# Kernel optimization log

Measured on AMD Instinct MI355X. Metric: run time of the kernel, lower is better.

Reference implementation:

```python
import jax, jax.numpy as jnp
import numpy as np

ALPHA = 0.2  # leaky relu slope


def setup_inputs() -> dict:
    key = jax.random.key(0)
    k_h, k_adj, k_w, k_a = jax.random.split(key, 4)
    B, N, F_in, F_out, H = 4, 2048, 128, 64, 4
    h = jax.random.normal(k_h, (B, N, F_in), dtype=jnp.float32)
    adj = jax.random.randint(k_adj, (N, N), 0, 2).astype(jnp.float32)
    # xavier_uniform with gain=1.414 (as in reset_parameters)
    gain = 1.414
    lim_w = gain * np.sqrt(6.0 / (F_in + F_out))
    W = jax.random.uniform(k_w, (H, F_in, F_out), minval=-lim_w, maxval=lim_w, dtype=jnp.float32)
    lim_a = gain * np.sqrt(6.0 / (2 * F_out + 1))
    a = jax.random.uniform(k_a, (H, 2 * F_out, 1), minval=-lim_a, maxval=lim_a, dtype=jnp.float32)
    return {"h": h, "adj": adj, "W": W, "a": a}


def reference(h, adj, W, a):
    B, N, _ = h.shape
    F_out = W.shape[2]
    # per-head linear transform: [B, N, H, F_out]
    ht = jnp.einsum('hio,bni->bnho', W, h)
    # split attention vector into src/dst halves; a^T [h_i; h_j] = a_src.h_i + a_dst.h_j
    a_src = a[:, :F_out, 0]   # [H, F_out]
    a_dst = a[:, F_out:, 0]   # [H, F_out]
    e_src = jnp.einsum('bnho,ho->bnh', ht, a_src)  # score contribution of node i (rows)
    e_dst = jnp.einsum('bnho,ho->bnh', ht, a_dst)  # score contribution of node j (cols)
    e = e_src[:, :, None, :] + e_dst[:, None, :, :]           # [B, N, N, H]
    e = jnp.where(e >= 0, e, ALPHA * e)                        # leaky relu
    e = e + (-1e20 * (1.0 - adj))[None, :, :, None]            # adjacency mask (shared over batch/heads)
    att = jax.nn.softmax(e, axis=2)                            # softmax over neighbors j
    # dropout p=0.0 (eval-mode reference): identity
    h_prime = jnp.einsum('bmnh,bnho->bmho', att, ht)           # [B, N, H, F_out]
    return h_prime.reshape(B, N, -1)                           # concat heads -> [B, N, H*F_out]
```

## Files before the change

kernel.cpp:

```cpp
#include <hip/hip_runtime.h>

#define ALPHA 0.2f
#define LOG2E 1.44269504088896340736f

constexpr int BB  = 4;
constexpr int NN  = 2048;
constexpr int FIN = 128;
constexpr int FO  = 64;
constexpr int HH  = 4;
constexpr int CC  = BB * HH;

using half8   = __attribute__((ext_vector_type(8))) _Float16;
using floatx4 = __attribute__((ext_vector_type(4))) float;

__device__ __forceinline__ float fast_exp2(float x) {
#if __has_builtin(__builtin_amdgcn_exp2f)
  return __builtin_amdgcn_exp2f(x);
#else
  return exp2f(x);
#endif
}

union PK4 { _Float16 f[4]; uint2 u; };

__global__ __launch_bounds__(256) void gat_k12(
    const float* __restrict__ h, const float* __restrict__ W,
    const float* __restrict__ a, const float* __restrict__ adj,
    _Float16* __restrict__ htT, float* __restrict__ esrcT,
    float* __restrict__ edst, float* __restrict__ gpart,
    unsigned* __restrict__ adjbits) {
  const int blk = blockIdx.x;
  const int t = threadIdx.x;
  const int w = t >> 6, lane = t & 63;

  if (blk < 512) {
    const int m = blk * 4 + w;
    float areg[32];
    const float* arow = adj + (size_t)m * NN;
#pragma unroll
    for (int j = 0; j < 32; ++j) areg[j] = arow[j * 64 + lane];
#pragma unroll
    for (int j = 0; j < 32; ++j) {
      const unsigned long long mask = __ballot(areg[j] != 0.f);
      if (lane == 0) {
        adjbits[m * 64 + j * 2 + 0] = (unsigned)mask;
        adjbits[m * 64 + j * 2 + 1] = (unsigned)(mask >> 32);
      }
    }
    return;
  }

  const int pb = blk - 512;
  const int c  = (pb & 7) | (((pb >> 3) & 1) << 3);
  const int nt = pb >> 4;
  const int n0 = nt * 64;
  const int b = c >> 2, hh = c & 3;
  const int q = lane >> 4, r16 = lane & 15;

  __shared__ __align__(16) _Float16 Xs[64 * 128];
  __shared__ __align__(16) _Float16 WT[64 * 128];
  __shared__ float wasb[128];
  __shared__ float wadb[128];
  __shared__ float edsh[64];

  {
    const int k = t & 127;
    const float* wrow = W + ((size_t)hh * 128 + k) * 64;
    const float* av = a + hh * 128 + ((t >> 7) << 6);
    float s = 0.f;
#pragma unroll
    for (int o = 0; o < 16; ++o) {
      const float4 wv = *(const float4*)(wrow + o * 4);
      const float4 av4 = *(const float4*)(av + o * 4);
      s += wv.x * av4.x + wv.y * av4.y + wv.z * av4.z + wv.w * av4.w;
    }
    if (t < 128) wasb[k] = s; else wadb[k] = s;
  }

  {
    const int k = t >> 1, fh = (t & 1) * 32;
    const float* wsrc = W + ((size_t)hh * 128 + k) * 64 + fh;
    const int chunk = k >> 3, within = k & 7;
#pragma unroll
    for (int i = 0; i < 8; ++i) {
      const float4 v = *(const float4*)(wsrc + i * 4);
      const _Float16 f4[4] = {(_Float16)v.x, (_Float16)v.y,
                              (_Float16)v.z, (_Float16)v.w};
#pragma unroll
      for (int u = 0; u < 4; ++u) {
        const int f = fh + i * 4 + u;
        WT[f * 128 + ((chunk ^ (f & 15)) << 3) + within] = f4[u];
      }
    }
  }

  __syncthreads();

  {
    const int r = t >> 2, cq = t & 3;
    const float* hsrc = h + ((size_t)(b * NN + n0 + r)) * FIN + cq * 32;
    float es = 0.f, ed = 0.f;
#pragma unroll
    for (int i = 0; i < 8; ++i) {
      const float4 v = *(const float4*)(hsrc + i * 4);
      const float4 ws = *(const float4*)&wasb[cq * 32 + i * 4];
      const float4 wd = *(const float4*)&wadb[cq * 32 + i * 4];
      es += v.x * ws.x + v.y * ws.y + v.z * ws.z + v.w * ws.w;
      ed += v.x * wd.x + v.y * wd.y + v.z * wd.z + v.w * wd.w;
      PK4 pk;
      pk.f[0] = (_Float16)v.x; pk.f[1] = (_Float16)v.y;
      pk.f[2] = (_Float16)v.z; pk.f[3] = (_Float16)v.w;
      const int chunk = cq * 4 + (i >> 1);
      *(uint2*)&Xs[r * 128 + ((chunk ^ (r & 15)) << 3) + (i & 1) * 4] = pk.u;
    }
    es += __shfl_xor(es, 1, 64); es += __shfl_xor(es, 2, 64);
    ed += __shfl_xor(ed, 1, 64); ed += __shfl_xor(ed, 2, 64);
    if (cq == 0) {
      const float edl = ed * LOG2E;
      esrcT[(size_t)(n0 + r) * CC + c] = es * LOG2E;
      edst[(size_t)c * NN + n0 + r]    = edl;
      edsh[r] = edl;
    }
  }

  __syncthreads();

  if (t < 64) {
    float v = edsh[t];
#pragma unroll
    for (int off = 1; off < 64; off <<= 1) v = fmaxf(v, __shfl_xor(v, off, 64));
    if (t == 0) gpart[c * 32 + nt] = v;
  }

  floatx4 acc[4];
#pragma unroll
  for (int ft = 0; ft < 4; ++ft) acc[ft] = floatx4{0.f, 0.f, 0.f, 0.f};

  half8 afrag[4];
#pragma unroll
  for (int ks = 0; ks < 4; ++ks) {
    const int slot = (ks * 4 + q) ^ r16;
    afrag[ks] = *(const half8*)&Xs[(w * 16 + r16) * 128 + (slot << 3)];
  }
#pragma unroll
  for (int ks = 0; ks < 4; ++ks) {
#pragma unroll
    for (int ft = 0; ft < 4; ++ft) {
      const int fr = ft * 16 + r16;
      const int slot = (ks * 4 + q) ^ (fr & 15);
      const half8 bfrag = *(const half8*)&WT[fr * 128 + (slot << 3)];
      acc[ft] = __builtin_amdgcn_mfma_f32_16x16x32_f16(afrag[ks], bfrag,
                                                       acc[ft], 0, 0, 0);
    }
  }

#pragma unroll
  for (int ft = 0; ft < 4; ++ft) {
    PK4 pk;
#pragma unroll
    for (int x = 0; x < 4; ++x) pk.f[x] = (_Float16)acc[ft][x];
    const int fcol = ft * 16 + r16;
    const int n = n0 + w * 16 + q * 4;
    *(uint2*)(htT + ((size_t)c * FO + fcol) * NN + n) = pk.u;
  }
}

__global__ __launch_bounds__(1024, 8) void gat_k3_pv(
    const _Float16* __restrict__ htT, const float* __restrict__ esrcT,
    const float* __restrict__ edst, const unsigned* __restrict__ adjbits,
    const float* __restrict__ gpart, float* __restrict__ out) {
  const int blk0 = blockIdx.x;
  const int c  = (blk0 & 7) | (((blk0 >> 3) & 1) << 3);
  const int m0 = (blk0 >> 4) * 64;
  const int b = c >> 2, hh = c & 3;
  const int t = threadIdx.x;
  const int w = t >> 6;
  const int kg = w >> 2;
  const int wl = w & 3;
  const int lane = t & 63;
  const int q = lane >> 4, r16 = lane & 15;
  const int row = m0 + wl * 16 + r16;
  const int rl  = wl * 16 + r16;

  __shared__ __align__(16) char smem[81920];
  _Float16* Vt  = (_Float16*)smem;
  float* zzF    = (float*)(smem + 49152);
  unsigned* abL = (unsigned*)(smem + 65536);
  float* abuf   = (float*)smem;

  const _Float16* vsrc = htT + (size_t)c * FO * NN;

  const int f0 = t >> 4, sg0 = t & 15;
  const size_t goff0 = (size_t)f0 * NN + (size_t)((sg0 ^ (f0 & 15)) * 8);

#define STAGE(BUF, NBASE)                                                      \
  __builtin_amdgcn_global_load_lds(                                            \
      (const __attribute__((address_space(1))) void*)(vsrc + goff0 + (NBASE)), \
      (__attribute__((address_space(3))) void*)(smem + (BUF)*16384 + t*16),    \
      16, 0, 0)

  const float em = esrcT[(size_t)row * CC + c];
  const float2 edv = *(const float2*)(edst + (size_t)c * NN + t * 2);
  const uint4 abv = *(const uint4*)&adjbits[(size_t)(m0 + (t >> 4)) * 64 +
                                            (t & 15) * 4];
  float gv = gpart[c * 32 + (lane & 31)];

  {
    float4 zzv;
    zzv.x = fast_exp2(edv.x);
    zzv.y = fast_exp2(ALPHA * edv.x);
    zzv.z = fast_exp2(edv.y);
    zzv.w = fast_exp2(ALPHA * edv.y);
    *(float4*)&zzF[t * 4] = zzv;
  }
  *(uint4*)&abL[(t >> 4) * 64 + (((t & 15) ^ ((t >> 4) & 15)) << 2)] = abv;

#pragma unroll
  for (int off = 1; off < 32; off <<= 1)
    gv = fmaxf(gv, __shfl_xor(gv, off, 64));
  const float gm = gv;

  __syncthreads();

  const float s0r = em + gm;
  const float rm = (s0r >= 0.f) ? s0r : ALPHA * s0r;
  const float Am   = fast_exp2(em - rm);
  const float Bm   = fast_exp2(fmaf(ALPHA, em, -rm));
  const float Zthr = fast_exp2(-em);

  floatx4 acc[4];
#pragma unroll
  for (int ft = 0; ft < 4; ++ft) acc[ft] = floatx4{0.f, 0.f, 0.f, 0.f};
  floatx4 accs = floatx4{0.f, 0.f, 0.f, 0.f};

  half8 ones;
#pragma unroll
  for (int k = 0; k < 8; ++k) ones[k] = (_Float16)1.0f;

  STAGE(0, 0);
  STAGE(1, 128);

#pragma unroll
  for (int step = 0; step < 16; ++step) {
    const int bufs = step % 3;
    const unsigned bits =
        abL[rl * 64 + ((step ^ (rl & 15)) << 2) + kg] >> (q * 8);
    const int nb = step * 128 + kg * 32 + q * 8;
    float4 vz[4];
#pragma unroll
    for (int i = 0; i < 4; ++i) vz[i] = *(const float4*)&zzF[nb * 2 + i * 4];
    const float* zp = (const float*)vz;
    half8 afrag;
#pragma unroll
    for (int k = 0; k < 8; ++k) {
      const float z1 = zp[2 * k], z2 = zp[2 * k + 1];
      const bool sel = (z1 >= Zthr);
      const float zc = sel ? z1 : z2;
      const float cf = sel ? Am : Bm;
      float p = cf * zc;
      p = ((bits >> k) & 1u) ? p : 0.f;
      afrag[k] = (_Float16)p;
    }

    if (step < 15) {
      asm volatile("s_waitcnt vmcnt(1) lgkmcnt(0)" ::: "memory");
    } else {
      asm volatile("s_waitcnt vmcnt(0) lgkmcnt(0)" ::: "memory");
    }
    __builtin_amdgcn_s_barrier();
    asm volatile("" ::: "memory");

    if (step <= 13) STAGE((step + 2) % 3, (step + 2) * 128);

    const int bufo = bufs * 8192;
    __builtin_amdgcn_s_setprio(1);
    accs = __builtin_amdgcn_mfma_f32_16x16x32_f16(afrag, ones, accs, 0, 0, 0);
#pragma unroll
    for (int ft = 0; ft < 4; ++ft) {
      const int fr = ft * 16 + r16;
      const int oct = kg * 4 + q;
      const half8 bfrag =
          *(const half8*)&Vt[bufo + fr * 128 + ((oct ^ (fr & 15)) << 3)];
      acc[ft] = __builtin_amdgcn_mfma_f32_16x16x32_f16(afrag, bfrag,
                                                       acc[ft], 0, 0, 0);
    }
    __builtin_amdgcn_s_setprio(0);
  }

  __syncthreads();
  if (kg >= 1) {
    const int base = ((kg - 1) * 256 + (t & 255)) * 21;
#pragma unroll
    for (int ft = 0; ft < 4; ++ft)
#pragma unroll
      for (int x = 0; x < 4; ++x) abuf[base + ft * 4 + x] = acc[ft][x];
#pragma unroll
    for (int x = 0; x < 4; ++x) abuf[base + 16 + x] = accs[x];
  }
  __syncthreads();
  if (kg == 0) {
#pragma unroll
    for (int g = 0; g < 3; ++g) {
      const int base = (g * 256 + t) * 21;
#pragma unroll
      for (int ft = 0; ft < 4; ++ft)
#pragma unroll
        for (int x = 0; x < 4; ++x) acc[ft][x] += abuf[base + ft * 4 + x];
#pragma unroll
      for (int x = 0; x < 4; ++x) accs[x] += abuf[base + 16 + x];
    }
#pragma unroll
    for (int x = 0; x < 4; ++x) {
      const float rinv = 1.0f / accs[x];
      const int mrow = m0 + wl * 16 + q * 4 + x;
      float* op = out + ((size_t)b * NN + mrow) * 256 + hh * 64;
#pragma unroll
      for (int ft = 0; ft < 4; ++ft) op[ft * 16 + r16] = acc[ft][x] * rinv;
    }
  }
#undef STAGE
}

extern "C" void kernel_launch(void* const* d_in, const int* in_sizes, int n_in,
                              void* d_out, int out_size, void* d_ws, size_t ws_size,
                              hipStream_t stream) {
  const float* h   = (const float*)d_in[0];
  const float* adj = (const float*)d_in[1];
  const float* W   = (const float*)d_in[2];
  const float* a   = (const float*)d_in[3];
  float* out = (float*)d_out;

  char* ws = (char*)d_ws;
  _Float16* htT   = (_Float16*)(ws);
  float* esrcT    = (float*)(ws + 4 * 1024 * 1024);
  float* edst     = (float*)(ws + 4 * 1024 * 1024 + 131072);
  unsigned* abits = (unsigned*)(ws + 4 * 1024 * 1024 + 2 * 131072);
  float* gpart    = (float*)(ws + 4 * 1024 * 1024 + 2 * 131072 + 524288);

  gat_k12<<<dim3(1024), dim3(256), 0, stream>>>(h, W, a, adj, htT, esrcT,
                                                edst, gpart, abits);
  gat_k3_pv<<<dim3(CC * (NN / 64)), dim3(1024), 0, stream>>>(htT, esrcT, edst,
                                                             abits, gpart, out);
}
```

Before: 108.3 us.

## Fuse projection and attention kernels with a grid-wide atomic barrier

Merges the projection/adjacency-bitmask kernel and the attention PV kernel into one persistent launch of 512 blocks of 1024 threads. Warps 0-3 do the per-tile projection and warps 4-11 pack adjacency bits. A software grid barrier (atomic counter plus spin with sleep) then separates the phases before the attention work. This removes one kernel launch and its tail gap, but adds a memset, relies on all 512 blocks being co-resident, and leaves many threads idle during the first phase.

```diff
diff --git a/kernel.cpp b/kernel.cpp
--- a/kernel.cpp
+++ b/kernel.cpp
@@ -9,6 +9,7 @@
 constexpr int FO  = 64;
 constexpr int HH  = 4;
 constexpr int CC  = BB * HH;
+constexpr unsigned NBLK = 512;
 
 using half8   = __attribute__((ext_vector_type(8))) _Float16;
 using floatx4 = __attribute__((ext_vector_type(4))) float;
@@ -23,80 +24,83 @@
 
 union PK4 { _Float16 f[4]; uint2 u; };
 
-__global__ __launch_bounds__(256) void gat_k12(
+__global__ __launch_bounds__(1024, 8) void gat_fused(
     const float* __restrict__ h, const float* __restrict__ W,
     const float* __restrict__ a, const float* __restrict__ adj,
     _Float16* __restrict__ htT, float* __restrict__ esrcT,
     float* __restrict__ edst, float* __restrict__ gpart,
-    unsigned* __restrict__ adjbits) {
-  const int blk = blockIdx.x;
+    unsigned* __restrict__ adjbits, unsigned* __restrict__ bar,
+    float* __restrict__ out) {
+  const int blk0 = blockIdx.x;
+  const int c    = (blk0 & 7) | (((blk0 >> 3) & 1) << 3);
+  const int tile = blk0 >> 4;
+  const int b = c >> 2, hh = c & 3;
   const int t = threadIdx.x;
-  const int w = t >> 6, lane = t & 63;
-
-  if (blk < 512) {
-    const int m = blk * 4 + w;
-    float areg[32];
+  const int lane = t & 63;
+  const int q = lane >> 4, r16 = lane & 15;
+  const int n0 = tile * 64;
+
+  __shared__ __align__(16) char smem[81920];
+  _Float16* Xs  = (_Float16*)smem;
+  _Float16* WT  = (_Float16*)(smem + 16384);
+  float* wasb   = (float*)(smem + 32768);
+  float* wadb   = (float*)(smem + 33280);
+  float* edsh   = (float*)(smem + 33792);
+
+  if (t < 256) {
+    {
+      const int k = t & 127;
+      const float* wrow = W + ((size_t)hh * 128 + k) * 64;
+      const float* av = a + hh * 128 + ((t >> 7) << 6);
+      float s = 0.f;
+#pragma unroll
+      for (int o = 0; o < 16; ++o) {
+        const float4 wv = *(const float4*)(wrow + o * 4);
+        const float4 av4 = *(const float4*)(av + o * 4);
+        s += wv.x * av4.x + wv.y * av4.y + wv.z * av4.z + wv.w * av4.w;
+      }
+      if (t < 128) wasb[k] = s; else wadb[k] = s;
+    }
+    {
+      const int k = t >> 1, fh = (t & 1) * 32;
+      const float* wsrc = W + ((size_t)hh * 128 + k) * 64 + fh;
+      const int chunk = k >> 3, within = k & 7;
+#pragma unroll
+      for (int i = 0; i < 8; ++i) {
+        const float4 v = *(const float4*)(wsrc + i * 4);
+        const _Float16 f4[4] = {(_Float16)v.x, (_Float16)v.y,
+                                (_Float16)v.z, (_Float16)v.w};
+#pragma unroll
+        for (int u = 0; u < 4; ++u) {
+          const int f = fh + i * 4 + u;
+          WT[f * 128 + ((chunk ^ (f & 15)) << 3) + within] = f4[u];
+        }
+      }
+    }
+  } else if (t < 768) {
+    const int tb = t - 256;
+    const int wv = tb >> 6;
+    const int rowi = wv >> 1;
+    const int jb = (wv & 1) * 16;
+    const int l = tb & 63;
+    const int m = blk0 * 4 + rowi;
     const float* arow = adj + (size_t)m * NN;
-#pragma unroll
-    for (int j = 0; j < 32; ++j) areg[j] = arow[j * 64 + lane];
-#pragma unroll
-    for (int j = 0; j < 32; ++j) {
+    float areg[16];
+#pragma unroll
+    for (int j = 0; j < 16; ++j) areg[j] = arow[(jb + j) * 64 + l];
+#pragma unroll
+    for (int j = 0; j < 16; ++j) {
       const unsigned long long mask = __ballot(areg[j] != 0.f);
-      if (lane == 0) {
-        adjbits[m * 64 + j * 2 + 0] = (unsigned)mask;
-        adjbits[m * 64 + j * 2 + 1] = (unsigned)(mask >> 32);
+      if (l == 0) {
+        adjbits[m * 64 + (jb + j) * 2 + 0] = (unsigned)mask;
+        adjbits[m * 64 + (jb + j) * 2 + 1] = (unsigned)(mask >> 32);
       }
     }
-    return;
-  }
-
-  const int pb = blk - 512;
-  const int c  = (pb & 7) | (((pb >> 3) & 1) << 3);
-  const int nt = pb >> 4;
-  const int n0 = nt * 64;
-  const int b = c >> 2, hh = c & 3;
-  const int q = lane >> 4, r16 = lane & 15;
-
-  __shared__ __align__(16) _Float16 Xs[64 * 128];
-  __shared__ __align__(16) _Float16 WT[64 * 128];
-  __shared__ float wasb[128];
-  __shared__ float wadb[128];
-  __shared__ float edsh[64];
-
-  {
-    const int k = t & 127;
-    const float* wrow = W + ((size_t)hh * 128 + k) * 64;
-    const float* av = a + hh * 128 + ((t >> 7) << 6);
-    float s = 0.f;
-#pragma unroll
-    for (int o = 0; o < 16; ++o) {
-      const float4 wv = *(const float4*)(wrow + o * 4);
-      const float4 av4 = *(const float4*)(av + o * 4);
-      s += wv.x * av4.x + wv.y * av4.y + wv.z * av4.z + wv.w * av4.w;
-    }
-    if (t < 128) wasb[k] = s; else wadb[k] = s;
-  }
-
-  {
-    const int k = t >> 1, fh = (t & 1) * 32;
-    const float* wsrc = W + ((size_t)hh * 128 + k) * 64 + fh;
-    const int chunk = k >> 3, within = k & 7;
-#pragma unroll
-    for (int i = 0; i < 8; ++i) {
-      const float4 v = *(const float4*)(wsrc + i * 4);
-      const _Float16 f4[4] = {(_Float16)v.x, (_Float16)v.y,
-                              (_Float16)v.z, (_Float16)v.w};
-#pragma unroll
-      for (int u = 0; u < 4; ++u) {
-        const int f = fh + i * 4 + u;
-        WT[f * 128 + ((chunk ^ (f & 15)) << 3) + within] = f4[u];
-      }
-    }
-  }
-
-  __syncthreads();
-
-  {
+  }
+
+  __syncthreads();
+
+  if (t < 256) {
     const int r = t >> 2, cq = t & 3;
     const float* hsrc = h + ((size_t)(b * NN + n0 + r)) * FIN + cq * 32;
     float es = 0.f, ed = 0.f;
@@ -129,60 +133,61 @@
     float v = edsh[t];
 #pragma unroll
     for (int off = 1; off < 64; off <<= 1) v = fmaxf(v, __shfl_xor(v, off, 64));
-    if (t == 0) gpart[c * 32 + nt] = v;
-  }
-
-  floatx4 acc[4];
-#pragma unroll
-  for (int ft = 0; ft < 4; ++ft) acc[ft] = floatx4{0.f, 0.f, 0.f, 0.f};
-
-  half8 afrag[4];
-#pragma unroll
-  for (int ks = 0; ks < 4; ++ks) {
-    const int slot = (ks * 4 + q) ^ r16;
-    afrag[ks] = *(const half8*)&Xs[(w * 16 + r16) * 128 + (slot << 3)];
-  }
-#pragma unroll
-  for (int ks = 0; ks < 4; ++ks) {
+    if (t == 0) gpart[c * 32 + tile] = v;
+  }
+  if (t < 256) {
+    const int w1 = t >> 6;
+    floatx4 pacc[4];
+#pragma unroll
+    for (int ft = 0; ft < 4; ++ft) pacc[ft] = floatx4{0.f, 0.f, 0.f, 0.f};
+    half8 pafrag[4];
+#pragma unroll
+    for (int ks = 0; ks < 4; ++ks) {
+      const int slot = (ks * 4 + q) ^ r16;
+      pafrag[ks] = *(const half8*)&Xs[(w1 * 16 + r16) * 128 + (slot << 3)];
+    }
+#pragma unroll
+    for (int ks = 0; ks < 4; ++ks) {
+#pragma unroll
+      for (int ft = 0; ft < 4; ++ft) {
+        const int fr = ft * 16 + r16;
+        const int slot = (ks * 4 + q) ^ (fr & 15);
+        const half8 bfrag = *(const half8*)&WT[fr * 128 + (slot << 3)];
+        pacc[ft] = __builtin_amdgcn_mfma_f32_16x16x32_f16(pafrag[ks], bfrag,
+                                                          pacc[ft], 0, 0, 0);
+      }
+    }
 #pragma unroll
     for (int ft = 0; ft < 4; ++ft) {
-      const int fr = ft * 16 + r16;
-      const int slot = (ks * 4 + q) ^ (fr & 15);
-      const half8 bfrag = *(const half8*)&WT[fr * 128 + (slot << 3)];
-      acc[ft] = __builtin_amdgcn_mfma_f32_16x16x32_f16(afrag[ks], bfrag,
-                                                       acc[ft], 0, 0, 0);
-    }
-  }
-
-#pragma unroll
-  for (int ft = 0; ft < 4; ++ft) {
-    PK4 pk;
-#pragma unroll
-    for (int x = 0; x < 4; ++x) pk.f[x] = (_Float16)acc[ft][x];
-    const int fcol = ft * 16 + r16;
-    const int n = n0 + w * 16 + q * 4;
-    *(uint2*)(htT + ((size_t)c * FO + fcol) * NN + n) = pk.u;
-  }
-}
-
-__global__ __launch_bounds__(1024, 8) void gat_k3_pv(
-    const _Float16* __restrict__ htT, const float* __restrict__ esrcT,
-    const float* __restrict__ edst, const unsigned* __restrict__ adjbits,
-    const float* __restrict__ gpart, float* __restrict__ out) {
-  const int blk0 = blockIdx.x;
-  const int c  = (blk0 & 7) | (((blk0 >> 3) & 1) << 3);
-  const int m0 = (blk0 >> 4) * 64;
-  const int b = c >> 2, hh = c & 3;
-  const int t = threadIdx.x;
+      PK4 pk;
+#pragma unroll
+      for (int x = 0; x < 4; ++x) pk.f[x] = (_Float16)pacc[ft][x];
+      const int fcol = ft * 16 + r16;
+      const int n = n0 + w1 * 16 + q * 4;
+      *(uint2*)(htT + ((size_t)c * FO + fcol) * NN + n) = pk.u;
+    }
+  }
+
+  __syncthreads();
+  if (t == 0) {
+    __hip_atomic_fetch_add(bar, 1u, __ATOMIC_RELEASE,
+                           __HIP_MEMORY_SCOPE_AGENT);
+    unsigned v;
+    do {
+      __builtin_amdgcn_s_sleep(8);
+      v = __hip_atomic_load(bar, __ATOMIC_RELAXED, __HIP_MEMORY_SCOPE_AGENT);
+    } while (v < NBLK);
+  }
+  __syncthreads();
+  __builtin_amdgcn_fence(__ATOMIC_ACQUIRE, "agent");
+
+  const int m0 = tile * 64;
   const int w = t >> 6;
   const int kg = w >> 2;
   const int wl = w & 3;
-  const int lane = t & 63;
-  const int q = lane >> 4, r16 = lane & 15;
   const int row = m0 + wl * 16 + r16;
   const int rl  = wl * 16 + r16;
 
-  __shared__ __align__(16) char smem[81920];
   _Float16* Vt  = (_Float16*)smem;
   float* zzF    = (float*)(smem + 49152);
   unsigned* abL = (unsigned*)(smem + 65536);
@@ -336,9 +341,9 @@
   float* edst     = (float*)(ws + 4 * 1024 * 1024 + 131072);
   unsigned* abits = (unsigned*)(ws + 4 * 1024 * 1024 + 2 * 131072);
   float* gpart    = (float*)(ws + 4 * 1024 * 1024 + 2 * 131072 + 524288);
-
-  gat_k12<<<dim3(1024), dim3(256), 0, stream>>>(h, W, a, adj, htT, esrcT,
-                                                edst, gpart, abits);
-  gat_k3_pv<<<dim3(CC * (NN / 64)), dim3(1024), 0, stream>>>(htT, esrcT, edst,
-                                                             abits, gpart, out);
+  unsigned* bar   = (unsigned*)(ws + 4 * 1024 * 1024 + 2 * 131072 + 524288 + 4096);
+
+  (void)hipMemsetAsync(bar, 0, 128, stream);
+  gat_fused<<<dim3(NBLK), dim3(1024), 0, stream>>>(
+      h, W, a, adj, htT, esrcT, edst, gpart, abits, bar, out);
 }
```

New measurement: 219.6 us. +102.8%, slower.
